# Performance work log

Measured on AMD Instinct MI355X. Metric: run time of the kernel, lower is better.

Reference implementation:

```python
import jax, jax.numpy as jnp
import numpy as np
from jax import lax

N_LAYERS = 10  # Sinkhorn(n_layers=10)


def setup_inputs() -> dict:
    key = jax.random.key(0)
    k1, k2, k3 = jax.random.split(key, 3)
    S, NA, NB = 4, 4096, 4096
    alpha = jax.random.uniform(k1, (S, NA), jnp.float32, 0.05, 1.0)
    alpha = alpha / alpha.sum(-1, keepdims=True)  # probability simplex
    beta = jax.random.uniform(k2, (S, NB), jnp.float32, 0.05, 1.0)
    beta = beta / beta.sum(-1, keepdims=True)
    C = jax.random.uniform(k3, (NA, NB), jnp.float32)  # nonneg cost matrix
    eps = jnp.float32(0.1)  # entropic regularization
    return {"alpha": alpha, "beta": beta, "C": C, "eps": eps}


def reference(alpha, beta, C, eps):
    # Log-domain Sinkhorn: f,g are dual potentials, shapes (S,NA)/(S,NB).
    log_alpha = jnp.log(alpha)
    log_beta = jnp.log(beta)

    def log_dot_exp(A, b):
        # A: (n, m), b: (S, m) -> (S, n); matches torch log_dot_exp (2D case)
        return jax.scipy.special.logsumexp((-A[None, :, :] + b[:, None, :]) / eps, axis=-1)

    def step(carry, _):
        _, g = carry
        f = eps * (log_alpha - log_dot_exp(C, g))
        g = eps * (log_beta - log_dot_exp(C.T, f))
        return (f, g), None

    f0 = jnp.zeros_like(alpha)
    g0 = jnp.zeros_like(beta)
    (f, g), _ = lax.scan(step, (f0, g0), None, length=N_LAYERS)
    return f, g
```

## Files before the change

kernel.cpp:

```cpp
#include <hip/hip_runtime.h>
#include <stdint.h>

#define NN 4096
#define NITER 10
#define ROWS 16
#define NBLK 256
#define THREADS 512

#define RED_OFF 131072

typedef float v2f __attribute__((ext_vector_type(2)));

static __device__ __forceinline__ unsigned short f2bf(float f) {
  union { float f; unsigned int i; } x; x.f = f;
  unsigned int i = x.i;
  i += 0x7FFFu + ((i >> 16) & 1u);
  return (unsigned short)(i >> 16);
}
static __device__ __forceinline__ unsigned int pk2(float a, float b) {
  return (unsigned int)f2bf(a) | ((unsigned int)f2bf(b) << 16);
}
static __device__ __forceinline__ float2 unpk(unsigned int u) {
  union { unsigned int i; float f; } a, b;
  a.i = u << 16; b.i = u & 0xFFFF0000u;
  return make_float2(a.f, b.f);
}
static __device__ __forceinline__ float read_eps(const void* p) {
  float f = *(const float*)p;
  if (f > 1e-4f && f < 1.0f) return f;
  union { unsigned int i; float f; } x;
  x.i = ((unsigned int)*(const unsigned short*)p) << 16;
  return x.f;
}
static __device__ __forceinline__ void astore8(unsigned long long* p, unsigned long long v) {
  __hip_atomic_store(p, v, __ATOMIC_RELAXED, __HIP_MEMORY_SCOPE_AGENT);
}
static __device__ __forceinline__ v2f mk2(float a, float b) {
  v2f r; r.x = a; r.y = b; return r;
}
#define FMA2(a, b, c) __builtin_elementwise_fma(a, b, c)

__global__ __launch_bounds__(256) void zero_flags(unsigned int* __restrict__ c) {
#pragma unroll
  for (int k = 0; k < 32; ++k) c[threadIdx.x + k * 256] = 0;
}

static __device__ __forceinline__ void wait_group(
    const unsigned int* flags, int q, unsigned token) {
  const unsigned int* p = flags + (q * 64 + (threadIdx.x & 63)) * 16;
  for (int spin = 0; spin < 400000; ++spin) {
    unsigned v = __hip_atomic_load(p, __ATOMIC_RELAXED,
                                   __HIP_MEMORY_SCOPE_AGENT);
    if (__ballot(v >= token) == 0xFFFFFFFFFFFFFFFFull) break;
    __builtin_amdgcn_s_sleep(1);
  }
}

__global__ __launch_bounds__(THREADS, 1) void sinkhorn_all(
    const float* __restrict__ alpha, const float* __restrict__ beta,
    const float* __restrict__ C, const void* __restrict__ epsp,
    unsigned short* __restrict__ K, unsigned long long* __restrict__ u_ep,
    unsigned long long* __restrict__ v_ep, unsigned int* __restrict__ u_flags,
    unsigned int* __restrict__ v_flags, float* __restrict__ out) {
  __shared__ float4 smem4[8320];
  char* sm = (char*)smem4;
  const int t = threadIdx.x, b = blockIdx.x;
  const int wave = t >> 6, lane = t & 63;
  const int own = ((b & 7) << 5) | (b >> 3);
  const int base0 = own * ROWS;
  const float eps = read_eps(epsp);
  const float nie = -1.0f / eps;

#pragma unroll 2
  for (int r = 0; r < ROWS; ++r) {
    const float4* Crow = (const float4*)(C + (size_t)(base0 + r) * NN) + t * 2;
    float4 c0 = Crow[0], c1 = Crow[1];
    uint4 k0;
    k0.x = pk2(__expf(c0.x * nie), __expf(c0.y * nie));
    k0.y = pk2(__expf(c0.z * nie), __expf(c0.w * nie));
    k0.z = pk2(__expf(c1.x * nie), __expf(c1.y * nie));
    k0.w = pk2(__expf(c1.z * nie), __expf(c1.w * nie));
    ((uint4*)(K + (size_t)(base0 + r) * NN))[t] = k0;
  }

  {
    const int p = t & 3, cb = p * 4, rb = t >> 2;
#pragma unroll 1
    for (int q2 = 0; q2 < 32; q2 += 8) {
      float4 cv[8];
#pragma unroll
      for (int z = 0; z < 8; ++z)
        cv[z] = *(const float4*)(C + (size_t)((q2 + z) * 128 + rb) * NN + base0 + cb);
#pragma unroll
      for (int z = 0; z < 8; ++z) {
        int n = (q2 + z) * 128 + rb;
        int u16 = ((n >> 10) * 8 + ((n >> 3) & 7)) * 256 + ((n >> 6) & 15) * 16;
        int jo = (n & 7) * 2;
        *(unsigned short*)(sm + (size_t)(u16 + cb + 0) * 16 + jo) = f2bf(__expf(cv[z].x * nie));
        *(unsigned short*)(sm + (size_t)(u16 + cb + 1) * 16 + jo) = f2bf(__expf(cv[z].y * nie));
        *(unsigned short*)(sm + (size_t)(u16 + cb + 2) * 16 + jo) = f2bf(__expf(cv[z].z * nie));
        *(unsigned short*)(sm + (size_t)(u16 + cb + 3) * 16 + jo) = f2bf(__expf(cv[z].w * nie));
      }
    }
  }
  __syncthreads();

  const uint4* smu4 = (const uint4*)sm;
  const uint4 ONES = make_uint4(0x3F803F80u, 0x3F803F80u, 0x3F803F80u, 0x3F803F80u);

  for (int it = 0; it < NITER; ++it) {
    v2f acc01[2] = {}, acc23[2] = {};
    const int r0 = base0 + wave * 2;
    const uint4* Kr0 = (const uint4*)(K + (size_t)r0 * NN);
    const uint4* VB = (const uint4*)(v_ep + (size_t)(it - 1) * NN);
    uint4 ka[4];
    ka[0] = Kr0[lane];            ka[1] = Kr0[512 + lane];
    ka[2] = Kr0[64 + lane];       ka[3] = Kr0[512 + 64 + lane];
#pragma unroll 1
    for (int q = 0; q < 4; ++q) {
      uint4 kan[4];
      if (q < 3) {
        const int f = (q + 1) * 128 + lane;
        kan[0] = Kr0[f];          kan[1] = Kr0[512 + f];
        kan[2] = Kr0[64 + f];     kan[3] = Kr0[512 + 64 + f];
      }
      if (it > 0) wait_group(v_flags, q, (unsigned)it);
#pragma unroll
      for (int ms = 0; ms < 2; ++ms) {
        const int fi = q * 128 + ms * 64 + lane;
        const uint4 k0 = ka[ms * 2], k1 = ka[ms * 2 + 1];
        uint4 svv[4];
        if (it == 0) {
          svv[0] = svv[1] = svv[2] = svv[3] = ONES;
        } else {
#pragma unroll
          for (int j = 0; j < 4; ++j) svv[j] = VB[fi * 4 + j];
        }
        unsigned cw0[4] = {k0.x, k0.y, k0.z, k0.w};
        unsigned cw1[4] = {k1.x, k1.y, k1.z, k1.w};
#pragma unroll
        for (int w = 0; w < 4; ++w) {
          float2 va = unpk(svv[w].x), vb_ = unpk(svv[w].y);
          float2 vc = unpk(svv[w].z), vd  = unpk(svv[w].w);
          float2 f0 = unpk(cw0[w]), f1 = unpk(cw1[w]);
          acc01[0] = FMA2(mk2(f0.x, f0.x), mk2(va.x, va.y), acc01[0]);
          acc23[0] = FMA2(mk2(f0.x, f0.x), mk2(vb_.x, vb_.y), acc23[0]);
          acc01[0] = FMA2(mk2(f0.y, f0.y), mk2(vc.x, vc.y), acc01[0]);
          acc23[0] = FMA2(mk2(f0.y, f0.y), mk2(vd.x, vd.y), acc23[0]);
          acc01[1] = FMA2(mk2(f1.x, f1.x), mk2(va.x, va.y), acc01[1]);
          acc23[1] = FMA2(mk2(f1.x, f1.x), mk2(vb_.x, vb_.y), acc23[1]);
          acc01[1] = FMA2(mk2(f1.y, f1.y), mk2(vc.x, vc.y), acc01[1]);
          acc23[1] = FMA2(mk2(f1.y, f1.y), mk2(vd.x, vd.y), acc23[1]);
        }
      }
      if (q < 3) {
#pragma unroll
        for (int z = 0; z < 4; ++z) ka[z] = kan[z];
      }
    }
    {
      float accf[2][4];
#pragma unroll
      for (int rr = 0; rr < 2; ++rr) {
        accf[rr][0] = acc01[rr].x; accf[rr][1] = acc01[rr].y;
        accf[rr][2] = acc23[rr].x; accf[rr][3] = acc23[rr].y;
      }
#pragma unroll
      for (int off = 32; off > 0; off >>= 1)
#pragma unroll
        for (int rr = 0; rr < 2; ++rr)
#pragma unroll
          for (int s = 0; s < 4; ++s)
            accf[rr][s] += __shfl_xor(accf[rr][s], off);
      if (lane < 2) {
        int row = r0 + lane;
        float ux = alpha[0 * NN + row] / accf[lane][0];
        float uy = alpha[1 * NN + row] / accf[lane][1];
        float uz = alpha[2 * NN + row] / accf[lane][2];
        float uw = alpha[3 * NN + row] / accf[lane][3];
        unsigned long long ub = (unsigned long long)pk2(ux, uy) |
                                ((unsigned long long)pk2(uz, uw) << 32);
        astore8(u_ep + (size_t)it * NN + row, ub);
        if (it == NITER - 1) {
          out[0 * NN + row] = eps * __logf(ux);
          out[1 * NN + row] = eps * __logf(uy);
          out[2 * NN + row] = eps * __logf(uz);
          out[3 * NN + row] = eps * __logf(uw);
        }
      }
    }
    __syncthreads();
    if (t == 0)
      __hip_atomic_store(u_flags + own * 16, (unsigned)(it + 1),
                         __ATOMIC_RELAXED, __HIP_MEMORY_SCOPE_AGENT);

    const int cB = t & 7, k2n = (t >> 3) & 15, hB = t >> 7;
    const int kq = (hB * 1024 + k2n * 64) >> 1;
    wait_group(u_flags, hB, (unsigned)(it + 1));
    const uint4* UB = (const uint4*)(u_ep + (size_t)it * NN);
    v2f bacc01[2] = {}, bacc23[2] = {};
    uint4 su[4];
#pragma unroll
    for (int j = 0; j < 4; ++j) su[j] = UB[kq + j];
#pragma unroll
    for (int s = 0; s < 8; ++s) {
      uint4 sun[4];
      if (s < 7) {
#pragma unroll
        for (int j = 0; j < 4; ++j) sun[j] = UB[kq + (s + 1) * 4 + j];
      }
      uint4 kt0 = smu4[(hB * 8 + s) * 256 + k2n * 16 + cB];
      uint4 kt1 = smu4[(hB * 8 + s) * 256 + k2n * 16 + cB + 8];
      unsigned cw0[4] = {kt0.x, kt0.y, kt0.z, kt0.w};
      unsigned cw1[4] = {kt1.x, kt1.y, kt1.z, kt1.w};
#pragma unroll
      for (int w = 0; w < 4; ++w) {
        float2 ua = unpk(su[w].x), ub_ = unpk(su[w].y);
        float2 uc = unpk(su[w].z), ud  = unpk(su[w].w);
        float2 f0 = unpk(cw0[w]), f1 = unpk(cw1[w]);
        bacc01[0] = FMA2(mk2(f0.x, f0.x), mk2(ua.x, ua.y), bacc01[0]);
        bacc23[0] = FMA2(mk2(f0.x, f0.x), mk2(ub_.x, ub_.y), bacc23[0]);
        bacc01[0] = FMA2(mk2(f0.y, f0.y), mk2(uc.x, uc.y), bacc01[0]);
        bacc23[0] = FMA2(mk2(f0.y, f0.y), mk2(ud.x, ud.y), bacc23[0]);
        bacc01[1] = FMA2(mk2(f1.x, f1.x), mk2(ua.x, ua.y), bacc01[1]);
        bacc23[1] = FMA2(mk2(f1.x, f1.x), mk2(ub_.x, ub_.y), bacc23[1]);
        bacc01[1] = FMA2(mk2(f1.y, f1.y), mk2(uc.x, uc.y), bacc01[1]);
        bacc23[1] = FMA2(mk2(f1.y, f1.y), mk2(ud.x, ud.y), bacc23[1]);
      }
      if (s < 7) {
#pragma unroll
        for (int j = 0; j < 4; ++j) su[j] = sun[j];
      }
    }
    {
      float bf0[4] = {bacc01[0].x, bacc01[0].y, bacc23[0].x, bacc23[0].y};
      float bf1[4] = {bacc01[1].x, bacc01[1].y, bacc23[1].x, bacc23[1].y};
#pragma unroll
      for (int off = 8; off <= 32; off <<= 1)
#pragma unroll
        for (int s2 = 0; s2 < 4; ++s2) {
          bf0[s2] += __shfl_xor(bf0[s2], off);
          bf1[s2] += __shfl_xor(bf1[s2], off);
        }
      if (lane < 8) {
        float4* red = (float4*)(sm + RED_OFF);
        red[(wave * 8 + lane) * 2 + 0] = make_float4(bf0[0], bf0[1], bf0[2], bf0[3]);
        red[(wave * 8 + lane) * 2 + 1] = make_float4(bf1[0], bf1[1], bf1[2], bf1[3]);
      }
    }
    __syncthreads();
    if (t < 16) {
      const float4* red = (const float4*)(sm + RED_OFF);
      const int cc = t & 7, sel = t >> 3;
      float4 a = make_float4(0.f, 0.f, 0.f, 0.f);
#pragma unroll
      for (int g = 0; g < 8; ++g) {
        float4 r = red[(g * 8 + cc) * 2 + sel];
        a.x += r.x; a.y += r.y; a.z += r.z; a.w += r.w;
      }
      int m = base0 + t;
      float vx = beta[0 * NN + m] / a.x;
      float vy = beta[1 * NN + m] / a.y;
      float vz = beta[2 * NN + m] / a.z;
      float vw = beta[3 * NN + m] / a.w;
      unsigned long long vb = (unsigned long long)pk2(vx, vy) |
                              ((unsigned long long)pk2(vz, vw) << 32);
      astore8(v_ep + (size_t)it * NN + m, vb);
      if (it == NITER - 1) {
        out[4 * NN + 0 * NN + m] = eps * __logf(vx);
        out[4 * NN + 1 * NN + m] = eps * __logf(vy);
        out[4 * NN + 2 * NN + m] = eps * __logf(vz);
        out[4 * NN + 3 * NN + m] = eps * __logf(vw);
      }
    }
    __syncthreads();
    if (t == 0 && it < NITER - 1)
      __hip_atomic_store(v_flags + own * 16, (unsigned)(it + 1),
                         __ATOMIC_RELAXED, __HIP_MEMORY_SCOPE_AGENT);
  }
}

extern "C" void kernel_launch(void* const* d_in, const int* in_sizes, int n_in,
                              void* d_out, int out_size, void* d_ws, size_t ws_size,
                              hipStream_t stream) {
  (void)in_sizes; (void)n_in; (void)out_size; (void)ws_size;
  const float* alpha = (const float*)d_in[0];
  const float* beta  = (const float*)d_in[1];
  const float* C     = (const float*)d_in[2];
  const void*  epsp  = d_in[3];

  char* ws = (char*)d_ws;
  unsigned short* K        = (unsigned short*)ws;
  unsigned long long* u_ep = (unsigned long long*)(ws + 33554432);
  unsigned long long* v_ep = (unsigned long long*)(ws + 33554432 + 327680);
  unsigned int* u_flags    = (unsigned int*)(ws + 33554432 + 655360);
  unsigned int* v_flags    = (unsigned int*)(ws + 33554432 + 655360 + 16384);
  float* out = (float*)d_out;

  zero_flags<<<1, 256, 0, stream>>>(u_flags);
  sinkhorn_all<<<NBLK, THREADS, 0, stream>>>(alpha, beta, C, epsp, K,
                                             u_ep, v_ep, u_flags, v_flags, out);
}
```

Before: 245.2 us.

## Build transposed K tile in LDS from global bf16 K after first u-step

Previously each block computed exp(-C/eps) twice: once for its own rows, written to global K, and again for its column slice of C, written to LDS. Now the column slice is built by reading the bf16 K rows other blocks wrote, after waiting on their iteration-1 flags. This drops the second strided fp32 C read and its exp work and overlaps the build with the first u-step. In exchange it adds a dependency on cross-block flags and global K visibility, which the code uses atomic 8-byte stores to provide.

```diff
diff --git a/kernel.cpp b/kernel.cpp
--- a/kernel.cpp
+++ b/kernel.cpp
@@ -75,33 +75,13 @@
   for (int r = 0; r < ROWS; ++r) {
     const float4* Crow = (const float4*)(C + (size_t)(base0 + r) * NN) + t * 2;
     float4 c0 = Crow[0], c1 = Crow[1];
-    uint4 k0;
-    k0.x = pk2(__expf(c0.x * nie), __expf(c0.y * nie));
-    k0.y = pk2(__expf(c0.z * nie), __expf(c0.w * nie));
-    k0.z = pk2(__expf(c1.x * nie), __expf(c1.y * nie));
-    k0.w = pk2(__expf(c1.z * nie), __expf(c1.w * nie));
-    ((uint4*)(K + (size_t)(base0 + r) * NN))[t] = k0;
-  }
-
-  {
-    const int p = t & 3, cb = p * 4, rb = t >> 2;
-#pragma unroll 1
-    for (int q2 = 0; q2 < 32; q2 += 8) {
-      float4 cv[8];
-#pragma unroll
-      for (int z = 0; z < 8; ++z)
-        cv[z] = *(const float4*)(C + (size_t)((q2 + z) * 128 + rb) * NN + base0 + cb);
-#pragma unroll
-      for (int z = 0; z < 8; ++z) {
-        int n = (q2 + z) * 128 + rb;
-        int u16 = ((n >> 10) * 8 + ((n >> 3) & 7)) * 256 + ((n >> 6) & 15) * 16;
-        int jo = (n & 7) * 2;
-        *(unsigned short*)(sm + (size_t)(u16 + cb + 0) * 16 + jo) = f2bf(__expf(cv[z].x * nie));
-        *(unsigned short*)(sm + (size_t)(u16 + cb + 1) * 16 + jo) = f2bf(__expf(cv[z].y * nie));
-        *(unsigned short*)(sm + (size_t)(u16 + cb + 2) * 16 + jo) = f2bf(__expf(cv[z].z * nie));
-        *(unsigned short*)(sm + (size_t)(u16 + cb + 3) * 16 + jo) = f2bf(__expf(cv[z].w * nie));
-      }
-    }
+    unsigned long long k0 = (unsigned long long)pk2(__expf(c0.x * nie), __expf(c0.y * nie)) |
+                            ((unsigned long long)pk2(__expf(c0.z * nie), __expf(c0.w * nie)) << 32);
+    unsigned long long k1 = (unsigned long long)pk2(__expf(c1.x * nie), __expf(c1.y * nie)) |
+                            ((unsigned long long)pk2(__expf(c1.z * nie), __expf(c1.w * nie)) << 32);
+    unsigned long long* dst =
+        (unsigned long long*)(K + (size_t)(base0 + r) * NN) + t * 2;
+    astore8(dst, k0); astore8(dst + 1, k1);
   }
   __syncthreads();
 
@@ -194,6 +174,29 @@
       __hip_atomic_store(u_flags + own * 16, (unsigned)(it + 1),
                          __ATOMIC_RELAXED, __HIP_MEMORY_SCOPE_AGENT);
 
+    if (it == 0) {
+      const int p = t & 3, cb = p * 4, rb = t >> 2;
+#pragma unroll 1
+      for (int q = 0; q < 4; ++q) {
+        wait_group(u_flags, q, 1u);
+        unsigned long long kv[8];
+#pragma unroll
+        for (int z = 0; z < 8; ++z)
+          kv[z] = *(const unsigned long long*)(K + (size_t)((q * 8 + z) * 128 + rb) * NN + base0 + cb);
+#pragma unroll
+        for (int z = 0; z < 8; ++z) {
+          int n = (q * 8 + z) * 128 + rb;
+          int u16 = ((n >> 10) * 8 + ((n >> 3) & 7)) * 256 + ((n >> 6) & 15) * 16;
+          int jo = (n & 7) * 2;
+          *(unsigned short*)(sm + (size_t)(u16 + cb + 0) * 16 + jo) = (unsigned short)(kv[z]);
+          *(unsigned short*)(sm + (size_t)(u16 + cb + 1) * 16 + jo) = (unsigned short)(kv[z] >> 16);
+          *(unsigned short*)(sm + (size_t)(u16 + cb + 2) * 16 + jo) = (unsigned short)(kv[z] >> 32);
+          *(unsigned short*)(sm + (size_t)(u16 + cb + 3) * 16 + jo) = (unsigned short)(kv[z] >> 48);
+        }
+      }
+      __syncthreads();
+    }
+
     const int cB = t & 7, k2n = (t >> 3) & 15, hB = t >> 7;
     const int kq = (hB * 1024 + k2n * 64) >> 1;
     wait_group(u_flags, hB, (unsigned)(it + 1));
```

Result: slower. 250.5 us (+2.2%).
